# Kernel optimization log

Measured on AMD Instinct MI355X. Metric: run time of the kernel, lower is better.

## Reference

```python
import jax, jax.numpy as jnp
import numpy as np

NUM_HEADS = 8
CHUNK = 2
TAU = 2.0

# --- LIF neuron with ATan surrogate gradient (spikingjelly MultiStepLIFNode, hard reset to 0, detach_reset) ---
@jax.custom_vjp
def spike(x):
    return (x >= 0.0).astype(x.dtype)

def _spike_fwd(x):
    return spike(x), x

def _spike_bwd(x, g):
    alpha = 2.0
    sg = (alpha / 2.0) / (1.0 + (jnp.pi / 2.0 * alpha * x) ** 2)
    return (g * sg,)

spike.defvjp(_spike_fwd, _spike_bwd)

def lif(x_seq, v_th=1.0):
    # x_seq: [T, ...]; v' = v + (x - v)/tau ; spike if v' >= v_th ; hard reset v=0 (reset path detached)
    def step(v, x):
        v = v + (x - v) / TAU
        s = spike(v - v_th)
        v = v * (1.0 - jax.lax.stop_gradient(s))
        return v, s
    _, s = jax.lax.scan(step, jnp.zeros_like(x_seq[0]), x_seq)
    return s

def conv1x1_bn(x, W, scale, bias, conv_bias=None):
    # 1x1 conv over channel dim + eval-mode BN (per-channel affine)
    y = jnp.einsum('tbchw,dc->tbdhw', x, W)
    if conv_bias is not None:
        y = y + conv_bias[None, None, :, None, None]
    return y * scale[None, None, :, None, None] + bias[None, None, :, None, None]


def setup_inputs() -> dict:
    key = jax.random.key(0)
    ks = jax.random.split(key, 16)
    T, B, C, H, W = 4, 32, 512, 16, 16
    s = 1.0 / np.sqrt(C)
    return {
        'x': jax.random.normal(ks[0], (T, B, C, H, W), jnp.float32),
        'Wq': jax.random.normal(ks[1], (C, C), jnp.float32) * s,
        'q_scale': jax.random.uniform(ks[2], (C,), jnp.float32, 0.5, 1.5),
        'q_bias': jax.random.normal(ks[3], (C,), jnp.float32) * 0.1,
        'Wk': jax.random.normal(ks[4], (C, C), jnp.float32) * s,
        'k_scale': jax.random.uniform(ks[5], (C,), jnp.float32, 0.5, 1.5),
        'k_bias': jax.random.normal(ks[6], (C,), jnp.float32) * 0.1,
        'Wv': jax.random.normal(ks[7], (C, C), jnp.float32) * s,
        'v_scale': jax.random.uniform(ks[8], (C,), jnp.float32, 0.5, 1.5),
        'v_bias': jax.random.normal(ks[9], (C,), jnp.float32) * 0.1,
        'Wp': jax.random.normal(ks[10], (C, C), jnp.float32) * s,
        'bp': jax.random.normal(ks[11], (C,), jnp.float32) * 0.1,
        'p_scale': jax.random.uniform(ks[12], (C,), jnp.float32, 0.5, 1.5),
        'p_bias': jax.random.normal(ks[13], (C,), jnp.float32) * 0.1,
    }


def reference(x, Wq, q_scale, q_bias, Wk, k_scale, k_bias, Wv, v_scale, v_bias, Wp, bp, p_scale, p_bias):
    T, B, C, H, W = x.shape
    N = H * W
    hd = C // NUM_HEADS
    identity = x

    xs = lif(x)  # shortcut_lif

    def qkv_branch(W_, sc, bi):
        y = lif(conv1x1_bn(xs, W_, sc, bi))           # [T,B,C,H,W] spikes
        # flatten(3).transpose(-1,-2).reshape(...heads...).permute == split C, swap N/hd
        return jnp.swapaxes(y.reshape(T, B, NUM_HEADS, hd, N), -1, -2)  # [T,B,h,N,hd]

    q = qkv_branch(Wq, q_scale, q_bias)
    k = qkv_branch(Wk, k_scale, k_bias)
    v = qkv_branch(Wv, v_scale, v_bias)

    # STAtten: temporal chunking, linear attention q @ (k^T v)
    scaling = 1.0 / H
    nc = T // CHUNK

    def to_chunks(y):  # [T,B,h,N,hd] -> [nc,B,h,CHUNK*N,hd]
        return (y.reshape(nc, CHUNK, B, NUM_HEADS, N, hd)
                 .transpose(0, 2, 3, 1, 4, 5)
                 .reshape(nc, B, NUM_HEADS, CHUNK * N, hd))

    qc, kc, vc = to_chunks(q), to_chunks(k), to_chunks(v)
    attn = jnp.einsum('nbhsd,nbhse->nbhde', kc, vc) * scaling   # [nc,B,h,hd,hd]
    out = jnp.einsum('nbhsd,nbhde->nbhse', qc, attn)            # [nc,B,h,CHUNK*N,hd]
    out = (out.reshape(nc, B, NUM_HEADS, CHUNK, N, hd)
              .transpose(0, 3, 1, 2, 4, 5)
              .reshape(T, B, NUM_HEADS, N, hd))

    x2 = jnp.swapaxes(out, -1, -2).reshape(T, B, C, N)          # [T,B,C,N]
    x2 = lif(x2, v_th=0.5).reshape(T, B, C, H, W)               # attn_lif

    x3 = conv1x1_bn(x2, Wp, p_scale, p_bias, conv_bias=bp)      # proj conv+BN
    return x3 + identity, v
```

## Files before the change

kernel.cpp:

```cpp
#include <hip/hip_runtime.h>

typedef unsigned short ushort_t;
typedef unsigned char u8;
typedef short bf16x8 __attribute__((ext_vector_type(8)));
typedef float f32x4 __attribute__((ext_vector_type(4)));

#define T_DIM 4
#define B_DIM 32
#define C_DIM 512
#define N_DIM 256

__device__ __forceinline__ float bf2f(ushort_t u) {
  union { unsigned int i; float f; } x;
  x.i = ((unsigned int)u) << 16;
  return x.f;
}
__device__ __forceinline__ ushort_t f2bf(float f) {
  unsigned int u = __float_as_uint(f);
  u = (u + 0x7FFFu + ((u >> 16) & 1u)) >> 16;
  return (ushort_t)u;
}

__global__ __launch_bounds__(256) void k0_split(
    const float* __restrict__ Wq, const float* __restrict__ Wk,
    const float* __restrict__ Wv, const float* __restrict__ Wp,
    ushort_t* __restrict__ Sqkv, ushort_t* __restrict__ Sp)
{
  int gid = blockIdx.x * 256 + threadIdx.x;
  int w = gid >> 15;
  int off = (gid & 32767) * 8;
  const float* src = (w == 0) ? Wq : ((w == 1) ? Wk : ((w == 2) ? Wv : Wp));
  ushort_t* dst = (w < 3) ? (Sqkv + (size_t)w * 3 * 262144) : Sp;
  float wv[8];
  *(float4*)&wv[0] = *(const float4*)(src + off);
  *(float4*)&wv[4] = *(const float4*)(src + off + 4);
  ushort_t hi[8], mi[8], lo[8];
#pragma unroll
  for (int i = 0; i < 8; i++) {
    float f = wv[i];
    ushort_t h = f2bf(f);  float r  = f - bf2f(h);
    ushort_t m = f2bf(r);  float r2 = r - bf2f(m);
    ushort_t l = f2bf(r2);
    hi[i] = h; mi[i] = m; lo[i] = l;
  }
  *(uint4*)(dst + off)              = *(uint4*)&hi[0];
  *(uint4*)(dst + 262144 + off)     = *(uint4*)&mi[0];
  *(uint4*)(dst + 2 * 262144 + off) = *(uint4*)&lo[0];
}

__global__ __launch_bounds__(256) void k1_shortcut_lif(
    const float* __restrict__ x, u8* __restrict__ xsT8)
{
  const int n0 = blockIdx.x * 64;
  const int c0 = blockIdx.y * 64;
  const int b  = blockIdx.z;
  __shared__ u8 sm[64][80];
  const int tid = threadIdx.x;
  const int r  = tid >> 2;
  const int j0 = (tid & 3) * 16;
  float v[16];
#pragma unroll
  for (int i = 0; i < 16; i++) v[i] = 0.f;
  for (int t = 0; t < T_DIM; t++) {
    const float* xp = x + ((((size_t)t * B_DIM + b) * C_DIM) + c0 + r) * N_DIM + n0 + j0;
    float xv[16];
    *(float4*)&xv[0]  = *(const float4*)xp;
    *(float4*)&xv[4]  = *(const float4*)(xp + 4);
    *(float4*)&xv[8]  = *(const float4*)(xp + 8);
    *(float4*)&xv[12] = *(const float4*)(xp + 12);
    __syncthreads();
#pragma unroll
    for (int i = 0; i < 16; i++) {
      float nv = v[i] + (xv[i] - v[i]) * 0.5f;
      bool s = (nv >= 1.0f);
      v[i] = s ? 0.f : nv;
      sm[j0 + i][r] = s ? (u8)1 : (u8)0;
    }
    __syncthreads();
    union { uint4 u; u8 b[16]; } ov;
#pragma unroll
    for (int i = 0; i < 16; i++) ov.b[i] = sm[r][j0 + i];
    u8* op = xsT8 + ((((size_t)t * B_DIM + b) * N_DIM) + n0 + r) * C_DIM + c0 + j0;
    *(uint4*)op = ov.u;
  }
}

__global__ __launch_bounds__(512, 4) void k2_qkv(
    const u8* __restrict__ xsT8, const ushort_t* __restrict__ Sqkv,
    const float* __restrict__ qsc, const float* __restrict__ qbi,
    const float* __restrict__ ksc, const float* __restrict__ kbi,
    const float* __restrict__ vsc, const float* __restrict__ vbi,
    u8* __restrict__ qs8, u8* __restrict__ ks8, float* __restrict__ vout)
{
  const int nt = blockIdx.x;
  const int mt = blockIdx.y;
  const int b  = blockIdx.z;
  const int branch = mt >> 3;
  const int mloc = (mt & 7) * 64;
  const ushort_t* Ws = Sqkv + (size_t)branch * 3 * 262144;
  const float* scp = (branch == 0) ? qsc : ((branch == 1) ? ksc : vsc);
  const float* bip = (branch == 0) ? qbi : ((branch == 1) ? kbi : vbi);

  __shared__ ushort_t As3[2][3][64][32];
  __shared__ ushort_t Bs[2][128][32];

  const int tid  = threadIdx.x;
  const int lane = tid & 63;
  const int wave = tid >> 6;
  const int wrow = (wave >> 1) * 16;
  const int wcol = (wave & 1) * 64;
  const int frow = lane & 15;
  const int fsl  = lane >> 4;

  const u8* Bb0 = xsT8 + ((size_t)b * N_DIM + nt * 128) * C_DIM;

  const int ach0 = tid;
  const int ap0 = ach0 >> 8, ar0 = (ach0 & 255) >> 2, asl0 = ach0 & 3;
  const int ach1 = tid + 512;
  const int ap1 = ach1 >> 8, ar1 = (ach1 & 255) >> 2, asl1 = ach1 & 3;
  const int brow = tid >> 1, bsl0 = (tid & 1) * 2;
  uint4 pa0, pa1, pb;

#define K2_LOAD(s_) { int t_ = (s_) >> 4; int kb_ = ((s_) & 15) * 32;                     \
    pa0 = *(const uint4*)(Ws + (size_t)ap0 * 262144 + (size_t)(mloc + ar0) * 512 + kb_ + asl0 * 8); \
    if (tid < 256) {                                                                       \
      pa1 = *(const uint4*)(Ws + (size_t)ap1 * 262144 + (size_t)(mloc + ar1) * 512 + kb_ + asl1 * 8); \
      pb  = *(const uint4*)(Bb0 + (size_t)t_ * B_DIM * N_DIM * C_DIM + (size_t)brow * 512 + kb_ + bsl0 * 8); \
    } }

#define K2_WRITE(buf_) {                                                                   \
    *(uint4*)&As3[buf_][ap0][ar0][(asl0 ^ ((ar0 >> 1) & 3)) * 8] = pa0;                    \
    if (tid < 256) {                                                                       \
      *(uint4*)&As3[buf_][ap1][ar1][(asl1 ^ ((ar1 >> 1) & 3)) * 8] = pa1;                  \
      union { uint4 u; u8 bb[16]; } rw_; rw_.u = pb;                                       \
      ushort_t tmp_[16];                                                                   \
      _Pragma("unroll") for (int z_ = 0; z_ < 16; z_++) tmp_[z_] = rw_.bb[z_] ? (ushort_t)0x3F80u : (ushort_t)0u; \
      int sw_ = (brow >> 1) & 3;                                                           \
      *(uint4*)&Bs[buf_][brow][((bsl0) ^ sw_) * 8]     = *(uint4*)&tmp_[0];                \
      *(uint4*)&Bs[buf_][brow][((bsl0 + 1) ^ sw_) * 8] = *(uint4*)&tmp_[8];                \
    } }

  f32x4 acc[4];
  float vst[16];
#pragma unroll
  for (int i = 0; i < 16; i++) vst[i] = 0.f;
#pragma unroll
  for (int i = 0; i < 4; i++) acc[i] = (f32x4){0.f, 0.f, 0.f, 0.f};

  const int crow0 = (lane >> 4) * 4;
  const int cn    = lane & 15;
  float sc4[4], bi4[4];
#pragma unroll
  for (int r = 0; r < 4; r++) {
    int c = mloc + wrow + crow0 + r;
    sc4[r] = scp[c]; bi4[r] = bip[c];
  }

  K2_LOAD(0); K2_WRITE(0); __syncthreads();

  for (int s = 0; s < 64; s++) {
    const int cur = s & 1;
    if (s < 63) K2_LOAD(s + 1);
    bf16x8 bfr[4];
#pragma unroll
    for (int j = 0; j < 4; j++) {
      int row = wcol + j * 16 + frow;
      bfr[j] = *(const bf16x8*)&Bs[cur][row][(fsl ^ ((row >> 1) & 3)) * 8];
    }
    int arow = wrow + frow;
    int asw  = (fsl ^ ((arow >> 1) & 3)) * 8;
#pragma unroll
    for (int p = 0; p < 3; p++) {
      bf16x8 af = *(const bf16x8*)&As3[cur][p][arow][asw];
#pragma unroll
      for (int j = 0; j < 4; j++)
        acc[j] = __builtin_amdgcn_mfma_f32_16x16x32_bf16(af, bfr[j], acc[j], 0, 0, 0);
    }
    if (s < 63) K2_WRITE((s + 1) & 1);
    __syncthreads();

    if ((s & 15) == 15) {
      const int t = s >> 4;
      const size_t tb = (size_t)t * B_DIM + b;
      if (branch < 2) {
        u8* dst = (branch == 0) ? qs8 : ks8;
#pragma unroll
        for (int r = 0; r < 4; r++) {
          int c = mloc + wrow + crow0 + r;
#pragma unroll
          for (int j = 0; j < 4; j++) {
            int n = nt * 128 + wcol + j * 16 + cn;
            float y = acc[j][r] * sc4[r] + bi4[r];
            int vi = j * 4 + r;
            float v = vst[vi];
            v = v + (y - v) * 0.5f;
            bool sp = (v >= 1.0f);
            vst[vi] = sp ? 0.f : v;
            dst[(tb * C_DIM + c) * N_DIM + n] = sp ? (u8)1 : (u8)0;
          }
        }
      } else {
        const int hv = mloc >> 6;
        const int d0 = wrow + crow0;
#pragma unroll
        for (int j = 0; j < 4; j++) {
          int n = nt * 128 + wcol + j * 16 + cn;
          float4 o;
          float ov[4];
#pragma unroll
          for (int r = 0; r < 4; r++) {
            float y = acc[j][r] * sc4[r] + bi4[r];
            int vi = j * 4 + r;
            float v = vst[vi];
            v = v + (y - v) * 0.5f;
            bool sp = (v >= 1.0f);
            vst[vi] = sp ? 0.f : v;
            ov[r] = sp ? 1.0f : 0.0f;
          }
          o.x = ov[0]; o.y = ov[1]; o.z = ov[2]; o.w = ov[3];
          *(float4*)(vout + ((tb * 8 + hv) * N_DIM + n) * 64 + d0) = o;
        }
      }
#pragma unroll
      for (int i = 0; i < 4; i++) acc[i] = (f32x4){0.f, 0.f, 0.f, 0.f};
    }
  }
#undef K2_LOAD
#undef K2_WRITE
}

__global__ __launch_bounds__(256) void k3_attn(
    const u8* __restrict__ ks8, const float* __restrict__ vsp,
    float* __restrict__ attn)
{
  const int h  = blockIdx.x;
  const int b  = blockIdx.y;
  const int ch = blockIdx.z;
  __shared__ u8 KtT[64][80];
  __shared__ u8 Vt[64][80];
  const int tid = threadIdx.x;
  const int d0 = (tid >> 4) * 4;
  const int e0 = (tid & 15) * 4;
  float a[16];
#pragma unroll
  for (int i = 0; i < 16; i++) a[i] = 0.f;

  for (int tt = 0; tt < 2; tt++) {
    int t = ch * 2 + tt;
    for (int n0 = 0; n0 < 256; n0 += 64) {
      __syncthreads();
      {
        int d  = tid >> 2;
        int s0 = (tid & 3) * 16;
        union { uint4 u; u8 bvec[16]; } kb;
        kb.u = *(const uint4*)(ks8 + ((((size_t)t * B_DIM + b) * C_DIM) + h * 64 + d) * N_DIM + n0 + s0);
#pragma unroll
        for (int i = 0; i < 16; i++) KtT[s0 + i][d] = kb.bvec[i];
      }
      {
        const float* vb = vsp + ((((size_t)t * B_DIM + b) * 8 + h) * N_DIM + n0) * 64;
#pragma unroll
        for (int u = 0; u < 4; u++) {
          int chunk = tid + u * 256;
          int row = chunk >> 4;
          int eo  = (chunk & 15) * 4;
          float4 v4 = *(const float4*)(vb + (size_t)row * 64 + eo);
          Vt[row][eo + 0] = (u8)(v4.x != 0.f);
          Vt[row][eo + 1] = (u8)(v4.y != 0.f);
          Vt[row][eo + 2] = (u8)(v4.z != 0.f);
          Vt[row][eo + 3] = (u8)(v4.w != 0.f);
        }
      }
      __syncthreads();
      for (int s = 0; s < 64; s++) {
        uchar4 kb = *(const uchar4*)&KtT[s][d0];
        float kv[4] = { (float)kb.x, (float)kb.y, (float)kb.z, (float)kb.w };
        uchar4 vr = *(const uchar4*)&Vt[s][e0];
        float vv[4] = { (float)vr.x, (float)vr.y, (float)vr.z, (float)vr.w };
#pragma unroll
        for (int i = 0; i < 4; i++)
#pragma unroll
          for (int j = 0; j < 4; j++) a[i * 4 + j] += kv[i] * vv[j];
      }
    }
  }
  float* ap = attn + ((((size_t)ch * B_DIM + b) * 8 + h) * 64 + d0) * 64 + e0;
#pragma unroll
  for (int i = 0; i < 4; i++)
#pragma unroll
    for (int j = 0; j < 4; j++)
      ap[i * 64 + j] = a[i * 4 + j] * 0.0625f;
}

__global__ __launch_bounds__(256) void k4_out_lif(
    const u8* __restrict__ qs8, const float* __restrict__ attn,
    u8* __restrict__ x2sT8)
{
  const int h  = blockIdx.x;
  const int b  = blockIdx.y;
  const int nc = blockIdx.z;
  __shared__ float At[64][68];
  __shared__ u8 Qt[64][80];
  const int tid = threadIdx.x;
  const int e0 = (tid >> 4) * 4;
  const int n0 = (tid & 15) * 4;
  float vst[16];
#pragma unroll
  for (int i = 0; i < 16; i++) vst[i] = 0.f;

  for (int t = 0; t < T_DIM; t++) {
    if ((t & 1) == 0) {
      __syncthreads();
      const float* ap = attn + ((((size_t)(t >> 1) * B_DIM + b) * 8) + h) * 4096;
      int dr = tid >> 2;
      int co = (tid & 3) * 16;
#pragma unroll
      for (int u = 0; u < 4; u++)
        *(float4*)&At[dr][co + u * 4] = *(const float4*)(ap + dr * 64 + co + u * 4);
    }
    __syncthreads();
    {
      int d  = tid >> 2;
      int so = (tid & 3) * 16;
      *(uint4*)&Qt[d][so] =
        *(const uint4*)(qs8 + ((((size_t)t * B_DIM + b) * C_DIM) + h * 64 + d) * N_DIM + nc * 64 + so);
    }
    __syncthreads();
    float acc[16];
#pragma unroll
    for (int i = 0; i < 16; i++) acc[i] = 0.f;
    for (int d = 0; d < 64; d++) {
      float4 av = *(const float4*)&At[d][e0];
      float avv[4] = { av.x, av.y, av.z, av.w };
      uchar4 qr = *(const uchar4*)&Qt[d][n0];
      float qv[4] = { (float)qr.x, (float)qr.y, (float)qr.z, (float)qr.w };
#pragma unroll
      for (int i = 0; i < 4; i++)
#pragma unroll
        for (int j = 0; j < 4; j++) acc[i * 4 + j] += avv[i] * qv[j];
    }
#pragma unroll
    for (int j = 0; j < 4; j++) {
      u8 sv[4];
#pragma unroll
      for (int i = 0; i < 4; i++) {
        int vi = i * 4 + j;
        float y = acc[i * 4 + j];
        float nv = vst[vi] + (y - vst[vi]) * 0.5f;
        bool s = (nv >= 0.5f);
        vst[vi] = s ? 0.f : nv;
        sv[i] = s ? (u8)1 : (u8)0;
      }
      int n = nc * 64 + n0 + j;
      u8* op = x2sT8 + ((((size_t)t * B_DIM + b) * N_DIM) + n) * C_DIM + h * 64 + e0;
      *(uchar4*)op = make_uchar4(sv[0], sv[1], sv[2], sv[3]);
    }
  }
}

__global__ __launch_bounds__(512, 4) void k5_proj(
    const u8* __restrict__ x2sT8, const ushort_t* __restrict__ Sp,
    const float* __restrict__ bp, const float* __restrict__ psc,
    const float* __restrict__ pbi,
    const float* __restrict__ x, float* __restrict__ out0)
{
  const int nt = blockIdx.x;
  const int mt = blockIdx.y;
  const int tb = blockIdx.z;
  const int mloc = mt * 64;

  __shared__ ushort_t As3[2][3][64][32];
  __shared__ ushort_t Bs[2][128][32];

  const int tid  = threadIdx.x;
  const int lane = tid & 63;
  const int wave = tid >> 6;
  const int wrow = (wave >> 1) * 16;
  const int wcol = (wave & 1) * 64;
  const int frow = lane & 15;
  const int fsl  = lane >> 4;

  const u8* Bb = x2sT8 + ((size_t)tb * N_DIM + nt * 128) * C_DIM;

  const int ach0 = tid;
  const int ap0 = ach0 >> 8, ar0 = (ach0 & 255) >> 2, asl0 = ach0 & 3;
  const int ach1 = tid + 512;
  const int ap1 = ach1 >> 8, ar1 = (ach1 & 255) >> 2, asl1 = ach1 & 3;
  const int brow = tid >> 1, bsl0 = (tid & 1) * 2;
  uint4 pa0, pa1, pb;

#define K5_LOAD(s_) { int kb_ = (s_) * 32;                                                 \
    pa0 = *(const uint4*)(Sp + (size_t)ap0 * 262144 + (size_t)(mloc + ar0) * 512 + kb_ + asl0 * 8); \
    if (tid < 256) {                                                                       \
      pa1 = *(const uint4*)(Sp + (size_t)ap1 * 262144 + (size_t)(mloc + ar1) * 512 + kb_ + asl1 * 8); \
      pb  = *(const uint4*)(Bb + (size_t)brow * 512 + kb_ + bsl0 * 8);                     \
    } }

#define K5_WRITE(buf_) {                                                                   \
    *(uint4*)&As3[buf_][ap0][ar0][(asl0 ^ ((ar0 >> 1) & 3)) * 8] = pa0;                    \
    if (tid < 256) {                                                                       \
      *(uint4*)&As3[buf_][ap1][ar1][(asl1 ^ ((ar1 >> 1) & 3)) * 8] = pa1;                  \
      union { uint4 u; u8 bb[16]; } rw_; rw_.u = pb;                                       \
      ushort_t tmp_[16];                                                                   \
      _Pragma("unroll") for (int z_ = 0; z_ < 16; z_++) tmp_[z_] = rw_.bb[z_] ? (ushort_t)0x3F80u : (ushort_t)0u; \
      int sw_ = (brow >> 1) & 3;                                                           \
      *(uint4*)&Bs[buf_][brow][((bsl0) ^ sw_) * 8]     = *(uint4*)&tmp_[0];                \
      *(uint4*)&Bs[buf_][brow][((bsl0 + 1) ^ sw_) * 8] = *(uint4*)&tmp_[8];                \
    } }

  f32x4 acc[4];
#pragma unroll
  for (int i = 0; i < 4; i++) acc[i] = (f32x4){0.f, 0.f, 0.f, 0.f};

  K5_LOAD(0); K5_WRITE(0); __syncthreads();

  for (int s = 0; s < 16; s++) {
    const int cur = s & 1;
    if (s < 15) K5_LOAD(s + 1);
    bf16x8 bfr[4];
#pragma unroll
    for (int j = 0; j < 4; j++) {
      int row = wcol + j * 16 + frow;
      bfr[j] = *(const bf16x8*)&Bs[cur][row][(fsl ^ ((row >> 1) & 3)) * 8];
    }
    int arow = wrow + frow;
    int asw  = (fsl ^ ((arow >> 1) & 3)) * 8;
#pragma unroll
    for (int p = 0; p < 3; p++) {
      bf16x8 af = *(const bf16x8*)&As3[cur][p][arow][asw];
#pragma unroll
      for (int j = 0; j < 4; j++)
        acc[j] = __builtin_amdgcn_mfma_f32_16x16x32_bf16(af, bfr[j], acc[j], 0, 0, 0);
    }
    if (s < 15) K5_WRITE((s + 1) & 1);
    __syncthreads();
  }

  const int crow0 = (lane >> 4) * 4;
  const int cn    = lane & 15;
#pragma unroll
  for (int r = 0; r < 4; r++) {
    int c = mloc + wrow + crow0 + r;
    float scf = psc[c];
    float bif = pbi[c];
    float bpf = bp[c];
#pragma unroll
    for (int j = 0; j < 4; j++) {
      int n = nt * 128 + wcol + j * 16 + cn;
      size_t idx = ((size_t)tb * C_DIM + c) * N_DIM + n;
      out0[idx] = (acc[j][r] + bpf) * scf + bif + x[idx];
    }
  }
#undef K5_LOAD
#undef K5_WRITE
}

extern "C" void kernel_launch(void* const* d_in, const int* in_sizes, int n_in,
                              void* d_out, int out_size, void* d_ws, size_t ws_size,
                              hipStream_t stream) {
  const float* x   = (const float*)d_in[0];
  const float* Wq  = (const float*)d_in[1];
  const float* qsc = (const float*)d_in[2];
  const float* qbi = (const float*)d_in[3];
  const float* Wk  = (const float*)d_in[4];
  const float* ksc = (const float*)d_in[5];
  const float* kbi = (const float*)d_in[6];
  const float* Wv  = (const float*)d_in[7];
  const float* vsc = (const float*)d_in[8];
  const float* vbi = (const float*)d_in[9];
  const float* Wp  = (const float*)d_in[10];
  const float* bp  = (const float*)d_in[11];
  const float* psc = (const float*)d_in[12];
  const float* pbi = (const float*)d_in[13];

  float* out0 = (float*)d_out;
  float* out1 = out0 + 16777216;

  const size_t M16 = 16u * 1024u * 1024u;
  char* o0 = (char*)d_out;
  char* ws = (char*)d_ws;

  u8*       xsT8  = (u8*)(o0);
  u8*       qs8   = (u8*)(o0 + M16);
  u8*       ks8   = (u8*)(o0 + 2 * M16);
  ushort_t* Sqkv  = (ushort_t*)(o0 + 3 * M16);
  float*    attn  = (float*)(o0);
  u8*       x2sT8 = (u8*)(ws);
  ushort_t* Sp    = (ushort_t*)(ws + M16);

  hipLaunchKernelGGL(k0_split,        dim3(512),        dim3(256), 0, stream,
                     Wq, Wk, Wv, Wp, Sqkv, Sp);
  hipLaunchKernelGGL(k1_shortcut_lif, dim3(4, 8, 32),   dim3(256), 0, stream, x, xsT8);
  hipLaunchKernelGGL(k2_qkv,          dim3(2, 24, 32),  dim3(512), 0, stream,
                     xsT8, Sqkv, qsc, qbi, ksc, kbi, vsc, vbi, qs8, ks8, out1);
  hipLaunchKernelGGL(k3_attn,         dim3(8, 32, 2),   dim3(256), 0, stream, ks8, out1, attn);
  hipLaunchKernelGGL(k4_out_lif,      dim3(8, 32, 4),   dim3(256), 0, stream, qs8, attn, x2sT8);
  hipLaunchKernelGGL(k5_proj,         dim3(2, 8, 128),  dim3(512), 0, stream,
                     x2sT8, Sp, bp, psc, pbi, x, out0);
}
```

Before: 524.2 us.

## Two-stage register prefetch in GEMMs and split attention reduction per timestep

The k2 and k5 GEMM main loops are unrolled by two and hold two register sets of prefetched tiles. This lets global loads for step s+2/s+3 be issued further ahead. The full __syncthreads is replaced with a raw lgkmcnt wait plus s_barrier, which does not wait on outstanding global loads. k3_attn now launches one block per timestep instead of per chunk, writing partial k^T v products that k4 sums pairwise when it loads them, which doubles parallelism in k3 at the cost of extra reads in k4.

```diff
diff --git a/kernel.cpp b/kernel.cpp
--- a/kernel.cpp
+++ b/kernel.cpp
@@ -19,6 +19,9 @@
   unsigned int u = __float_as_uint(f);
   u = (u + 0x7FFFu + ((u >> 16) & 1u)) >> 16;
   return (ushort_t)u;
+}
+__device__ __forceinline__ void sync_lds() {
+  asm volatile("s_waitcnt lgkmcnt(0)\ns_barrier" ::: "memory");
 }
 
 __global__ __launch_bounds__(256) void k0_split(
@@ -114,25 +117,26 @@
 
   const u8* Bb0 = xsT8 + ((size_t)b * N_DIM + nt * 128) * C_DIM;
 
-  const int ach0 = tid;
-  const int ap0 = ach0 >> 8, ar0 = (ach0 & 255) >> 2, asl0 = ach0 & 3;
+  const int ap0 = tid >> 8, ar0 = (tid & 255) >> 2, asl0 = tid & 3;
   const int ach1 = tid + 512;
   const int ap1 = ach1 >> 8, ar1 = (ach1 & 255) >> 2, asl1 = ach1 & 3;
   const int brow = tid >> 1, bsl0 = (tid & 1) * 2;
-  uint4 pa0, pa1, pb;
-
-#define K2_LOAD(s_) { int t_ = (s_) >> 4; int kb_ = ((s_) & 15) * 32;                     \
-    pa0 = *(const uint4*)(Ws + (size_t)ap0 * 262144 + (size_t)(mloc + ar0) * 512 + kb_ + asl0 * 8); \
-    if (tid < 256) {                                                                       \
-      pa1 = *(const uint4*)(Ws + (size_t)ap1 * 262144 + (size_t)(mloc + ar1) * 512 + kb_ + asl1 * 8); \
-      pb  = *(const uint4*)(Bb0 + (size_t)t_ * B_DIM * N_DIM * C_DIM + (size_t)brow * 512 + kb_ + bsl0 * 8); \
+
+  uint4 pa0_0, pa1_0, pb_0;
+  uint4 pa0_1, pa1_1, pb_1;
+
+#define K2_LOAD(s_, A0, A1, PB) { int t_ = (s_) >> 4; int kb_ = ((s_) & 15) * 32;          \
+    A0 = *(const uint4*)(Ws + (size_t)ap0 * 262144 + (size_t)(mloc + ar0) * 512 + kb_ + asl0 * 8); \
+    if (tid < 256) {                                                                        \
+      A1 = *(const uint4*)(Ws + (size_t)ap1 * 262144 + (size_t)(mloc + ar1) * 512 + kb_ + asl1 * 8); \
+      PB = *(const uint4*)(Bb0 + (size_t)t_ * B_DIM * N_DIM * C_DIM + (size_t)brow * 512 + kb_ + bsl0 * 8); \
     } }
 
-#define K2_WRITE(buf_) {                                                                   \
-    *(uint4*)&As3[buf_][ap0][ar0][(asl0 ^ ((ar0 >> 1) & 3)) * 8] = pa0;                    \
-    if (tid < 256) {                                                                       \
-      *(uint4*)&As3[buf_][ap1][ar1][(asl1 ^ ((ar1 >> 1) & 3)) * 8] = pa1;                  \
-      union { uint4 u; u8 bb[16]; } rw_; rw_.u = pb;                                       \
+#define K2_WRITE(buf_, A0, A1, PB) {                                                       \
+    *(uint4*)&As3[buf_][ap0][ar0][(asl0 ^ ((ar0 >> 1) & 3)) * 8] = A0;                     \
+    if (tid < 256) {                                                                        \
+      *(uint4*)&As3[buf_][ap1][ar1][(asl1 ^ ((ar1 >> 1) & 3)) * 8] = A1;                   \
+      union { uint4 u; u8 bb[16]; } rw_; rw_.u = PB;                                       \
       ushort_t tmp_[16];                                                                   \
       _Pragma("unroll") for (int z_ = 0; z_ < 16; z_++) tmp_[z_] = rw_.bb[z_] ? (ushort_t)0x3F80u : (ushort_t)0u; \
       int sw_ = (brow >> 1) & 3;                                                           \
@@ -140,6 +144,53 @@
       *(uint4*)&Bs[buf_][brow][((bsl0 + 1) ^ sw_) * 8] = *(uint4*)&tmp_[8];                \
     } }
 
+#define K2_MFMA(buf_) {                                                                    \
+    bf16x8 bfr_[4];                                                                        \
+    _Pragma("unroll") for (int j_ = 0; j_ < 4; j_++) {                                     \
+      int row_ = wcol + j_ * 16 + frow;                                                    \
+      bfr_[j_] = *(const bf16x8*)&Bs[buf_][row_][(fsl ^ ((row_ >> 1) & 3)) * 8]; }         \
+    int arow_ = wrow + frow; int asw_ = (fsl ^ ((arow_ >> 1) & 3)) * 8;                    \
+    _Pragma("unroll") for (int p_ = 0; p_ < 3; p_++) {                                     \
+      bf16x8 af_ = *(const bf16x8*)&As3[buf_][p_][arow_][asw_];                            \
+      _Pragma("unroll") for (int j_ = 0; j_ < 4; j_++)                                     \
+        acc[j_] = __builtin_amdgcn_mfma_f32_16x16x32_bf16(af_, bfr_[j_], acc[j_], 0, 0, 0); } }
+
+#define K2_EPI(t_) {                                                                       \
+    const size_t tb_ = (size_t)(t_) * B_DIM + b;                                           \
+    if (branch < 2) {                                                                      \
+      u8* dst_ = (branch == 0) ? qs8 : ks8;                                                \
+      _Pragma("unroll") for (int r_ = 0; r_ < 4; r_++) {                                   \
+        int c_ = mloc + wrow + crow0 + r_;                                                 \
+        _Pragma("unroll") for (int j_ = 0; j_ < 4; j_++) {                                 \
+          int n_ = nt * 128 + wcol + j_ * 16 + cn;                                         \
+          float y_ = acc[j_][r_] * sc4[r_] + bi4[r_];                                      \
+          int vi_ = j_ * 4 + r_;                                                           \
+          float v_ = vst[vi_];                                                             \
+          v_ = v_ + (y_ - v_) * 0.5f;                                                      \
+          bool sp_ = (v_ >= 1.0f);                                                         \
+          vst[vi_] = sp_ ? 0.f : v_;                                                       \
+          dst_[(tb_ * C_DIM + c_) * N_DIM + n_] = sp_ ? (u8)1 : (u8)0;                     \
+        } }                                                                                \
+    } else {                                                                               \
+      const int hv_ = mloc >> 6;                                                           \
+      const int d0_ = wrow + crow0;                                                        \
+      _Pragma("unroll") for (int j_ = 0; j_ < 4; j_++) {                                   \
+        int n_ = nt * 128 + wcol + j_ * 16 + cn;                                           \
+        float ov_[4];                                                                      \
+        _Pragma("unroll") for (int r_ = 0; r_ < 4; r_++) {                                 \
+          float y_ = acc[j_][r_] * sc4[r_] + bi4[r_];                                      \
+          int vi_ = j_ * 4 + r_;                                                           \
+          float v_ = vst[vi_];                                                             \
+          v_ = v_ + (y_ - v_) * 0.5f;                                                      \
+          bool sp_ = (v_ >= 1.0f);                                                         \
+          vst[vi_] = sp_ ? 0.f : v_;                                                       \
+          ov_[r_] = sp_ ? 1.0f : 0.0f;                                                     \
+        }                                                                                  \
+        float4 o_; o_.x = ov_[0]; o_.y = ov_[1]; o_.z = ov_[2]; o_.w = ov_[3];             \
+        *(float4*)(vout + ((tb_ * 8 + hv_) * N_DIM + n_) * 64 + d0_) = o_;                 \
+      } }                                                                                  \
+    _Pragma("unroll") for (int i_ = 0; i_ < 4; i_++) acc[i_] = (f32x4){0.f, 0.f, 0.f, 0.f}; }
+
   f32x4 acc[4];
   float vst[16];
 #pragma unroll
@@ -156,86 +207,36 @@
     sc4[r] = scp[c]; bi4[r] = bip[c];
   }
 
-  K2_LOAD(0); K2_WRITE(0); __syncthreads();
-
-  for (int s = 0; s < 64; s++) {
-    const int cur = s & 1;
-    if (s < 63) K2_LOAD(s + 1);
-    bf16x8 bfr[4];
-#pragma unroll
-    for (int j = 0; j < 4; j++) {
-      int row = wcol + j * 16 + frow;
-      bfr[j] = *(const bf16x8*)&Bs[cur][row][(fsl ^ ((row >> 1) & 3)) * 8];
-    }
-    int arow = wrow + frow;
-    int asw  = (fsl ^ ((arow >> 1) & 3)) * 8;
-#pragma unroll
-    for (int p = 0; p < 3; p++) {
-      bf16x8 af = *(const bf16x8*)&As3[cur][p][arow][asw];
-#pragma unroll
-      for (int j = 0; j < 4; j++)
-        acc[j] = __builtin_amdgcn_mfma_f32_16x16x32_bf16(af, bfr[j], acc[j], 0, 0, 0);
-    }
-    if (s < 63) K2_WRITE((s + 1) & 1);
-    __syncthreads();
-
-    if ((s & 15) == 15) {
-      const int t = s >> 4;
-      const size_t tb = (size_t)t * B_DIM + b;
-      if (branch < 2) {
-        u8* dst = (branch == 0) ? qs8 : ks8;
-#pragma unroll
-        for (int r = 0; r < 4; r++) {
-          int c = mloc + wrow + crow0 + r;
-#pragma unroll
-          for (int j = 0; j < 4; j++) {
-            int n = nt * 128 + wcol + j * 16 + cn;
-            float y = acc[j][r] * sc4[r] + bi4[r];
-            int vi = j * 4 + r;
-            float v = vst[vi];
-            v = v + (y - v) * 0.5f;
-            bool sp = (v >= 1.0f);
-            vst[vi] = sp ? 0.f : v;
-            dst[(tb * C_DIM + c) * N_DIM + n] = sp ? (u8)1 : (u8)0;
-          }
-        }
-      } else {
-        const int hv = mloc >> 6;
-        const int d0 = wrow + crow0;
-#pragma unroll
-        for (int j = 0; j < 4; j++) {
-          int n = nt * 128 + wcol + j * 16 + cn;
-          float4 o;
-          float ov[4];
-#pragma unroll
-          for (int r = 0; r < 4; r++) {
-            float y = acc[j][r] * sc4[r] + bi4[r];
-            int vi = j * 4 + r;
-            float v = vst[vi];
-            v = v + (y - v) * 0.5f;
-            bool sp = (v >= 1.0f);
-            vst[vi] = sp ? 0.f : v;
-            ov[r] = sp ? 1.0f : 0.0f;
-          }
-          o.x = ov[0]; o.y = ov[1]; o.z = ov[2]; o.w = ov[3];
-          *(float4*)(vout + ((tb * 8 + hv) * N_DIM + n) * 64 + d0) = o;
-        }
-      }
-#pragma unroll
-      for (int i = 0; i < 4; i++) acc[i] = (f32x4){0.f, 0.f, 0.f, 0.f};
-    }
+  K2_LOAD(0, pa0_0, pa1_0, pb_0);
+  K2_WRITE(0, pa0_0, pa1_0, pb_0);
+  K2_LOAD(1, pa0_1, pa1_1, pb_1);
+  __syncthreads();
+
+  for (int ss = 0; ss < 32; ss++) {
+    const int s0 = ss * 2;
+    if (s0 + 2 < 64) K2_LOAD(s0 + 2, pa0_0, pa1_0, pb_0);
+    K2_WRITE(1, pa0_1, pa1_1, pb_1);
+    K2_MFMA(0);
+    sync_lds();
+    if (s0 + 3 < 64) K2_LOAD(s0 + 3, pa0_1, pa1_1, pb_1);
+    if (s0 + 2 < 64) K2_WRITE(0, pa0_0, pa1_0, pb_0);
+    K2_MFMA(1);
+    if (((s0 + 1) & 15) == 15) K2_EPI((s0 + 1) >> 4);
+    sync_lds();
   }
 #undef K2_LOAD
 #undef K2_WRITE
+#undef K2_MFMA
+#undef K2_EPI
 }
 
 __global__ __launch_bounds__(256) void k3_attn(
     const u8* __restrict__ ks8, const float* __restrict__ vsp,
-    float* __restrict__ attn)
+    float* __restrict__ attn_part)
 {
-  const int h  = blockIdx.x;
-  const int b  = blockIdx.y;
-  const int ch = blockIdx.z;
+  const int h = blockIdx.x;
+  const int b = blockIdx.y;
+  const int t = blockIdx.z;
   __shared__ u8 KtT[64][80];
   __shared__ u8 Vt[64][80];
   const int tid = threadIdx.x;
@@ -245,46 +246,43 @@
 #pragma unroll
   for (int i = 0; i < 16; i++) a[i] = 0.f;
 
-  for (int tt = 0; tt < 2; tt++) {
-    int t = ch * 2 + tt;
-    for (int n0 = 0; n0 < 256; n0 += 64) {
-      __syncthreads();
-      {
-        int d  = tid >> 2;
-        int s0 = (tid & 3) * 16;
-        union { uint4 u; u8 bvec[16]; } kb;
-        kb.u = *(const uint4*)(ks8 + ((((size_t)t * B_DIM + b) * C_DIM) + h * 64 + d) * N_DIM + n0 + s0);
-#pragma unroll
-        for (int i = 0; i < 16; i++) KtT[s0 + i][d] = kb.bvec[i];
+  for (int n0 = 0; n0 < 256; n0 += 64) {
+    __syncthreads();
+    {
+      int d  = tid >> 2;
+      int s0 = (tid & 3) * 16;
+      union { uint4 u; u8 bvec[16]; } kb;
+      kb.u = *(const uint4*)(ks8 + ((((size_t)t * B_DIM + b) * C_DIM) + h * 64 + d) * N_DIM + n0 + s0);
+#pragma unroll
+      for (int i = 0; i < 16; i++) KtT[s0 + i][d] = kb.bvec[i];
+    }
+    {
+      const float* vb = vsp + ((((size_t)t * B_DIM + b) * 8 + h) * N_DIM + n0) * 64;
+#pragma unroll
+      for (int u = 0; u < 4; u++) {
+        int chunk = tid + u * 256;
+        int row = chunk >> 4;
+        int eo  = (chunk & 15) * 4;
+        float4 v4 = *(const float4*)(vb + (size_t)row * 64 + eo);
+        Vt[row][eo + 0] = (u8)(v4.x != 0.f);
+        Vt[row][eo + 1] = (u8)(v4.y != 0.f);
+        Vt[row][eo + 2] = (u8)(v4.z != 0.f);
+        Vt[row][eo + 3] = (u8)(v4.w != 0.f);
       }
-      {
-        const float* vb = vsp + ((((size_t)t * B_DIM + b) * 8 + h) * N_DIM + n0) * 64;
-#pragma unroll
-        for (int u = 0; u < 4; u++) {
-          int chunk = tid + u * 256;
-          int row = chunk >> 4;
-          int eo  = (chunk & 15) * 4;
-          float4 v4 = *(const float4*)(vb + (size_t)row * 64 + eo);
-          Vt[row][eo + 0] = (u8)(v4.x != 0.f);
-          Vt[row][eo + 1] = (u8)(v4.y != 0.f);
-          Vt[row][eo + 2] = (u8)(v4.z != 0.f);
-          Vt[row][eo + 3] = (u8)(v4.w != 0.f);
-        }
-      }
-      __syncthreads();
-      for (int s = 0; s < 64; s++) {
-        uchar4 kb = *(const uchar4*)&KtT[s][d0];
-        float kv[4] = { (float)kb.x, (float)kb.y, (float)kb.z, (float)kb.w };
-        uchar4 vr = *(const uchar4*)&Vt[s][e0];
-        float vv[4] = { (float)vr.x, (float)vr.y, (float)vr.z, (float)vr.w };
-#pragma unroll
-        for (int i = 0; i < 4; i++)
-#pragma unroll
-          for (int j = 0; j < 4; j++) a[i * 4 + j] += kv[i] * vv[j];
-      }
-    }
-  }
-  float* ap = attn + ((((size_t)ch * B_DIM + b) * 8 + h) * 64 + d0) * 64 + e0;
+    }
+    __syncthreads();
+    for (int s = 0; s < 64; s++) {
+      uchar4 kb = *(const uchar4*)&KtT[s][d0];
+      float kv[4] = { (float)kb.x, (float)kb.y, (float)kb.z, (float)kb.w };
+      uchar4 vr = *(const uchar4*)&Vt[s][e0];
+      float vv[4] = { (float)vr.x, (float)vr.y, (float)vr.z, (float)vr.w };
+#pragma unroll
+      for (int i = 0; i < 4; i++)
+#pragma unroll
+        for (int j = 0; j < 4; j++) a[i * 4 + j] += kv[i] * vv[j];
+    }
+  }
+  float* ap = attn_part + (((size_t)t * B_DIM + b) * 8 + h) * 4096 + d0 * 64 + e0;
 #pragma unroll
   for (int i = 0; i < 4; i++)
 #pragma unroll
@@ -293,7 +291,7 @@
 }
 
 __global__ __launch_bounds__(256) void k4_out_lif(
-    const u8* __restrict__ qs8, const float* __restrict__ attn,
+    const u8* __restrict__ qs8, const float* __restrict__ attn_part,
     u8* __restrict__ x2sT8)
 {
   const int h  = blockIdx.x;
@@ -309,16 +307,21 @@
   for (int i = 0; i < 16; i++) vst[i] = 0.f;
 
   for (int t = 0; t < T_DIM; t++) {
+    __syncthreads();
     if ((t & 1) == 0) {
-      __syncthreads();
-      const float* ap = attn + ((((size_t)(t >> 1) * B_DIM + b) * 8) + h) * 4096;
+      const float* p0 = attn_part + (((size_t)t * B_DIM + b) * 8 + h) * 4096;
+      const float* p1 = p0 + (size_t)B_DIM * 8 * 4096;
       int dr = tid >> 2;
       int co = (tid & 3) * 16;
 #pragma unroll
-      for (int u = 0; u < 4; u++)
-        *(float4*)&At[dr][co + u * 4] = *(const float4*)(ap + dr * 64 + co + u * 4);
-    }
-    __syncthreads();
+      for (int u = 0; u < 4; u++) {
+        float4 a0 = *(const float4*)(p0 + dr * 64 + co + u * 4);
+        float4 a1 = *(const float4*)(p1 + dr * 64 + co + u * 4);
+        float4 sum; sum.x = a0.x + a1.x; sum.y = a0.y + a1.y;
+        sum.z = a0.z + a1.z; sum.w = a0.w + a1.w;
+        *(float4*)&At[dr][co + u * 4] = sum;
+      }
+    }
     {
       int d  = tid >> 2;
       int so = (tid & 3) * 16;
@@ -382,25 +385,26 @@
 
   const u8* Bb = x2sT8 + ((size_t)tb * N_DIM + nt * 128) * C_DIM;
 
-  const int ach0 = tid;
-  const int ap0 = ach0 >> 8, ar0 = (ach0 & 255) >> 2, asl0 = ach0 & 3;
+  const int ap0 = tid >> 8, ar0 = (tid & 255) >> 2, asl0 = tid & 3;
   const int ach1 = tid + 512;
   const int ap1 = ach1 >> 8, ar1 = (ach1 & 255) >> 2, asl1 = ach1 & 3;
   const int brow = tid >> 1, bsl0 = (tid & 1) * 2;
-  uint4 pa0, pa1, pb;
-
-#define K5_LOAD(s_) { int kb_ = (s_) * 32;                                                 \
-    pa0 = *(const uint4*)(Sp + (size_t)ap0 * 262144 + (size_t)(mloc + ar0) * 512 + kb_ + asl0 * 8); \
-    if (tid < 256) {                                                                       \
-      pa1 = *(const uint4*)(Sp + (size_t)ap1 * 262144 + (size_t)(mloc + ar1) * 512 + kb_ + asl1 * 8); \
-      pb  = *(const uint4*)(Bb + (size_t)brow * 512 + kb_ + bsl0 * 8);                     \
+
+  uint4 pa0_0, pa1_0, pb_0;
+  uint4 pa0_1, pa1_1, pb_1;
+
+#define K5_LOAD(s_, A0, A1, PB) { int kb_ = (s_) * 32;                                     \
+    A0 = *(const uint4*)(Sp + (size_t)ap0 * 262144 + (size_t)(mloc + ar0) * 512 + kb_ + asl0 * 8); \
+    if (tid < 256) {                                                                        \
+      A1 = *(const uint4*)(Sp + (size_t)ap1 * 262144 + (size_t)(mloc + ar1) * 512 + kb_ + asl1 * 8); \
+      PB = *(const uint4*)(Bb + (size_t)brow * 512 + kb_ + bsl0 * 8);                      \
     } }
 
-#define K5_WRITE(buf_) {                                                                   \
-    *(uint4*)&As3[buf_][ap0][ar0][(asl0 ^ ((ar0 >> 1) & 3)) * 8] = pa0;                    \
-    if (tid < 256) {                                                                       \
-      *(uint4*)&As3[buf_][ap1][ar1][(asl1 ^ ((ar1 >> 1) & 3)) * 8] = pa1;                  \
-      union { uint4 u; u8 bb[16]; } rw_; rw_.u = pb;                                       \
+#define K5_WRITE(buf_, A0, A1, PB) {                                                       \
+    *(uint4*)&As3[buf_][ap0][ar0][(asl0 ^ ((ar0 >> 1) & 3)) * 8] = A0;                     \
+    if (tid < 256) {                                                                        \
+      *(uint4*)&As3[buf_][ap1][ar1][(asl1 ^ ((ar1 >> 1) & 3)) * 8] = A1;                   \
+      union { uint4 u; u8 bb[16]; } rw_; rw_.u = PB;                                       \
       ushort_t tmp_[16];                                                                   \
       _Pragma("unroll") for (int z_ = 0; z_ < 16; z_++) tmp_[z_] = rw_.bb[z_] ? (ushort_t)0x3F80u : (ushort_t)0u; \
       int sw_ = (brow >> 1) & 3;                                                           \
@@ -408,32 +412,36 @@
       *(uint4*)&Bs[buf_][brow][((bsl0 + 1) ^ sw_) * 8] = *(uint4*)&tmp_[8];                \
     } }
 
+#define K5_MFMA(buf_) {                                                                    \
+    bf16x8 bfr_[4];                                                                        \
+    _Pragma("unroll") for (int j_ = 0; j_ < 4; j_++) {                                     \
+      int row_ = wcol + j_ * 16 + frow;                                                    \
+      bfr_[j_] = *(const bf16x8*)&Bs[buf_][row_][(fsl ^ ((row_ >> 1) & 3)) * 8]; }         \
+    int arow_ = wrow + frow; int asw_ = (fsl ^ ((arow_ >> 1) & 3)) * 8;                    \
+    _Pragma("unroll") for (int p_ = 0; p_ < 3; p_++) {                                     \
+      bf16x8 af_ = *(const bf16x8*)&As3[buf_][p_][arow_][asw_];                            \
+      _Pragma("unroll") for (int j_ = 0; j_ < 4; j_++)                                     \
+        acc[j_] = __builtin_amdgcn_mfma_f32_16x16x32_bf16(af_, bfr_[j_], acc[j_], 0, 0, 0); } }
+
   f32x4 acc[4];
 #pragma unroll
   for (int i = 0; i < 4; i++) acc[i] = (f32x4){0.f, 0.f, 0.f, 0.f};
 
-  K5_LOAD(0); K5_WRITE(0); __syncthreads();
-
-  for (int s = 0; s < 16; s++) {
-    const int cur = s & 1;
-    if (s < 15) K5_LOAD(s + 1);
-    bf16x8 bfr[4];
-#pragma unroll
-    for (int j = 0; j < 4; j++) {
-      int row = wcol + j * 16 + frow;
-      bfr[j] = *(const bf16x8*)&Bs[cur][row][(fsl ^ ((row >> 1) & 3)) * 8];
-    }
-    int arow = wrow + frow;
-    int asw  = (fsl ^ ((arow >> 1) & 3)) * 8;
-#pragma unroll
-    for (int p = 0; p < 3; p++) {
-      bf16x8 af = *(const bf16x8*)&As3[cur][p][arow][asw];
-#pragma unroll
-      for (int j = 0; j < 4; j++)
-        acc[j] = __builtin_amdgcn_mfma_f32_16x16x32_bf16(af, bfr[j], acc[j], 0, 0, 0);
-    }
-    if (s < 15) K5_WRITE((s + 1) & 1);
-    __syncthreads();
+  K5_LOAD(0, pa0_0, pa1_0, pb_0);
+  K5_WRITE(0, pa0_0, pa1_0, pb_0);
+  K5_LOAD(1, pa0_1, pa1_1, pb_1);
+  __syncthreads();
+
+  for (int ss = 0; ss < 8; ss++) {
+    const int s0 = ss * 2;
+    if (s0 + 2 < 16) K5_LOAD(s0 + 2, pa0_0, pa1_0, pb_0);
+    K5_WRITE(1, pa0_1, pa1_1, pb_1);
+    K5_MFMA(0);
+    sync_lds();
+    if (s0 + 3 < 16) K5_LOAD(s0 + 3, pa0_1, pa1_1, pb_1);
+    if (s0 + 2 < 16) K5_WRITE(0, pa0_0, pa1_0, pb_0);
+    K5_MFMA(1);
+    sync_lds();
   }
 
   const int crow0 = (lane >> 4) * 4;
@@ -453,6 +461,7 @@
   }
 #undef K5_LOAD
 #undef K5_WRITE
+#undef K5_MFMA
 }
 
 extern "C" void kernel_launch(void* const* d_in, const int* in_sizes, int n_in,
@@ -484,7 +493,7 @@
   u8*       qs8   = (u8*)(o0 + M16);
   u8*       ks8   = (u8*)(o0 + 2 * M16);
   ushort_t* Sqkv  = (ushort_t*)(o0 + 3 * M16);
-  float*    attn  = (float*)(o0);
+  float*    attn_part = (float*)(o0);
   u8*       x2sT8 = (u8*)(ws);
   ushort_t* Sp    = (ushort_t*)(ws + M16);
 
@@ -493,8 +502,8 @@
   hipLaunchKernelGGL(k1_shortcut_lif, dim3(4, 8, 32),   dim3(256), 0, stream, x, xsT8);
   hipLaunchKernelGGL(k2_qkv,          dim3(2, 24, 32),  dim3(512), 0, stream,
                      xsT8, Sqkv, qsc, qbi, ksc, kbi, vsc, vbi, qs8, ks8, out1);
-  hipLaunchKernelGGL(k3_attn,         dim3(8, 32, 2),   dim3(256), 0, stream, ks8, out1, attn);
-  hipLaunchKernelGGL(k4_out_lif,      dim3(8, 32, 4),   dim3(256), 0, stream, qs8, attn, x2sT8);
+  hipLaunchKernelGGL(k3_attn,         dim3(8, 32, 4),   dim3(256), 0, stream, ks8, out1, attn_part);
+  hipLaunchKernelGGL(k4_out_lif,      dim3(8, 32, 4),   dim3(256), 0, stream, qs8, attn_part, x2sT8);
   hipLaunchKernelGGL(k5_proj,         dim3(2, 8, 128),  dim3(512), 0, stream,
                      x2sT8, Sp, bp, psc, pbi, x, out0);
 }
```

After: 588.7 us. +12.3%, slower.
